# Optimization experiments

Hardware: AMD Instinct MI355X
Metric: run time of the kernel (lower is better)

## Reference

```python
import jax, jax.numpy as jnp
from jax import lax
import numpy as np

DIM = 64
HEADS = 4
R = 8  # reduction_ratio: kv conv kernel == stride == R


def setup_inputs() -> dict:
    key = jax.random.key(0)
    k_x, k_q, k_kv, k_o = jax.random.split(key, 4)
    x = jax.random.normal(k_x, (2, DIM, 32, 64, 64), dtype=jnp.float32)
    # 1x1x1 conv weights stored as [out_c, in_c]
    w_q = jax.random.normal(k_q, (DIM, DIM), dtype=jnp.float32) * (1.0 / np.sqrt(DIM))
    # strided kv conv weights: [out_c=2*dim, in_c=dim, R, R, R]
    fan_in = DIM * R * R * R
    w_kv = jax.random.normal(k_kv, (2 * DIM, DIM, R, R, R), dtype=jnp.float32) * (1.0 / np.sqrt(fan_in))
    w_out = jax.random.normal(k_o, (DIM, DIM), dtype=jnp.float32) * (1.0 / np.sqrt(DIM))
    return {"x": x, "w_q": w_q, "w_kv": w_kv, "w_out": w_out}


def _attn(x, w_q, w_kv, w_out):
    B, C, D, H, W = x.shape
    hd = C // HEADS  # per-head channel dim
    scale = hd ** (-0.5)

    # to_q: 1x1x1 conv == channel mixing
    q = jnp.einsum('oc,bcdhw->bodhw', w_q, x)
    # to_kv: conv3d kernel=stride=R, no padding
    kv = lax.conv_general_dilated(
        x, w_kv, window_strides=(R, R, R), padding='VALID',
        dimension_numbers=('NCDHW', 'OIDHW', 'NCDHW'))
    k, v = jnp.split(kv, 2, axis=1)  # each [B, C, D/R, H/R, W/R]

    def to_seq(t):
        # 'b (h c) d x y -> (b h) (d x y) c'
        b, c_all, d, h, w = t.shape
        t = t.reshape(b, HEADS, hd, d * h * w)
        return t.transpose(0, 1, 3, 2).reshape(b * HEADS, d * h * w, hd)

    qs, ks, vs = to_seq(q), to_seq(k), to_seq(v)  # [(B*H), N, c], [(B*H), Nr, c]

    sim = jnp.einsum('bic,bjc->bij', qs, ks) * scale  # [(B*H), N, Nr]
    attn = jax.nn.softmax(sim, axis=-1)
    out = jnp.einsum('bij,bjc->bic', attn, vs)  # [(B*H), N, c]

    # '(b h) (d x y) c -> b (h c) d x y'
    out = out.reshape(B, HEADS, D * H * W, hd).transpose(0, 1, 3, 2)
    out = out.reshape(B, C, D, H, W)
    return jnp.einsum('oc,bcdhw->bodhw', w_out, out)


def reference(x, w_q, w_kv, w_out):
    return _attn(x, w_q, w_kv, w_out)
```

## Files before the change

kernel.cpp:

```cpp
#include <hip/hip_runtime.h>
#include <hip/hip_bf16.h>

#define NPOS 131072

typedef __attribute__((ext_vector_type(8))) short short8;
typedef __attribute__((ext_vector_type(4))) float floatx4;
typedef unsigned int uint32;

__device__ __forceinline__ unsigned short bf16b(float v) {
    __hip_bfloat16 h = __float2bfloat16(v);
    return __builtin_bit_cast(unsigned short, h);
}
__device__ __forceinline__ uint32 cvtpk(float lo, float hi) {
    uint32 r;
    asm("v_cvt_pk_bf16_f32 %0, %1, %2" : "=v"(r) : "v"(lo), "v"(hi));
    return r;
}
__device__ __forceinline__ uint32 pk2(float lo, float hi) {
    return (uint32)bf16b(lo) | ((uint32)bf16b(hi) << 16);
}
#if __has_builtin(__builtin_amdgcn_exp2f)
#define EXP2(x) __builtin_amdgcn_exp2f(x)
#else
#define EXP2(x) exp2f(x)
#endif
#if __has_builtin(__builtin_amdgcn_rcpf)
#define RCPF(x) __builtin_amdgcn_rcpf(x)
#else
#define RCPF(x) (1.0f / (x))
#endif

__device__ __forceinline__ short8 emb4(uint32 w0, uint32 w1) {
    union { uint32 u[4]; short8 s; } z;
    z.u[0] = w0; z.u[1] = w1; z.u[2] = 0; z.u[3] = 0;
    return z.s;
}
__device__ __forceinline__ short8 emb4m(const unsigned short* p) {
    uint32 w[2];
    __builtin_memcpy(w, p, 8);
    return emb4(w[0], w[1]);
}

__global__ void k_prep_w(const float* __restrict__ wq, const float* __restrict__ wout,
                         unsigned short* __restrict__ wqb, unsigned short* __restrict__ woutb) {
    const float QS = 0.36067376022224085f;
    int gid = blockIdx.x * 256 + threadIdx.x;
    wqb[gid]   = bf16b(wq[gid] * QS);
    woutb[gid] = bf16b(wout[gid]);
}

__global__ void k_prep_wkvb(const float* __restrict__ wkv, unsigned short* __restrict__ wtb) {
    int gid = blockIdx.x * 256 + threadIdx.x;
    int ic = gid >> 14;
    int oc = (gid >> 7) & 127;
    float4 v = *(const float4*)(wkv + ((size_t)(oc * 64 + ic)) * 512 + (size_t)(gid & 127) * 4);
    uint32* dst = (uint32*)(wtb + (size_t)gid * 4);
    dst[0] = cvtpk(v.x, v.y);
    dst[1] = cvtpk(v.z, v.w);
}

__global__ __launch_bounds__(256) void k_conv_mfma(const float* __restrict__ x,
                                                   const unsigned short* __restrict__ wtb,
                                                   float* __restrict__ partial) {
    __shared__ __align__(16) unsigned short As[64 * 72];
    __shared__ __align__(16) unsigned short Bs[128 * 72];
    const int bid = blockIdx.x;
    const int ic = bid & 63;
    const int b  = (bid >> 6) & 1;
    const int pz = bid >> 7;
    const int tid = threadIdx.x;
    const int lane = tid & 63, wv = tid >> 6;
    const int lc = lane & 15, lg = lane >> 4;

    floatx4 acc[4][2];
#pragma unroll
    for (int mt = 0; mt < 4; ++mt)
#pragma unroll
        for (int n = 0; n < 2; ++n) acc[mt][n] = {0.f, 0.f, 0.f, 0.f};

    const float* xp = x + ((size_t)b * 64 + ic) * NPOS + (size_t)pz * 8 * 4096;
    const unsigned short* wp = wtb + (size_t)ic * 128 * 512;

    for (int rz = 0; rz < 8; ++rz) {
        __syncthreads();
        const float* plane = xp + (size_t)rz * 4096;
#pragma unroll
        for (int t2 = 0; t2 < 4; ++t2) {
            int e = (t2 * 256 + tid) * 4;
            int y = e >> 6, x0 = e & 63;
            int p = ((y >> 3) << 3) + (x0 >> 3);
            int k = ((y & 7) << 3) + (x0 & 7);
            float4 v = *(const float4*)(plane + e);
            uint32* dst = (uint32*)&As[p * 72 + k];
            dst[0] = cvtpk(v.x, v.y);
            dst[1] = cvtpk(v.z, v.w);
        }
        {
            int oc = tid >> 1, hf = tid & 1;
            const uint4* src = (const uint4*)(wp + (size_t)oc * 512 + rz * 64 + hf * 32);
            uint4* dst = (uint4*)&Bs[oc * 72 + hf * 32];
#pragma unroll
            for (int r = 0; r < 4; ++r) dst[r] = src[r];
        }
        __syncthreads();
#pragma unroll
        for (int ks = 0; ks < 2; ++ks) {
            short8 bb0 = *(const short8*)&Bs[((wv * 2 + 0) * 16 + lc) * 72 + ks * 32 + lg * 8];
            short8 bb1 = *(const short8*)&Bs[((wv * 2 + 1) * 16 + lc) * 72 + ks * 32 + lg * 8];
#pragma unroll
            for (int mt = 0; mt < 4; ++mt) {
                short8 a = *(const short8*)&As[(mt * 16 + lc) * 72 + ks * 32 + lg * 8];
                acc[mt][0] = __builtin_amdgcn_mfma_f32_16x16x32_bf16(a, bb0, acc[mt][0], 0, 0, 0);
                acc[mt][1] = __builtin_amdgcn_mfma_f32_16x16x32_bf16(a, bb1, acc[mt][1], 0, 0, 0);
            }
        }
    }
    float* pb = partial + (((size_t)ic * 2 + b) * 256 + pz * 64) * 128;
#pragma unroll
    for (int mt = 0; mt < 4; ++mt)
#pragma unroll
        for (int ntl = 0; ntl < 2; ++ntl) {
            int oc = (wv * 2 + ntl) * 16 + lc;
#pragma unroll
            for (int r = 0; r < 4; ++r) {
                int m = mt * 16 + lg * 4 + r;
                pb[(size_t)m * 128 + oc] = acc[mt][ntl][r];
            }
        }
}

__global__ void k_reduce(const float* __restrict__ partial,
                         unsigned short* __restrict__ kt, unsigned short* __restrict__ vt) {
    int gid = blockIdx.x * 256 + threadIdx.x;
    int oc = gid & 127;
    int bp = gid >> 7;
    int b = bp >> 8;
    int j = bp & 255;
    const float* p = partial + (size_t)bp * 128 + oc;
    float s = 0.f;
#pragma unroll 8
    for (int ic = 0; ic < 64; ++ic) s += p[(size_t)ic * 65536];
    int h = (oc & 63) >> 4, i = oc & 15;
    if (oc < 64)
        kt[(((size_t)b * 4 + h) * 256 + j) * 16 + i] = bf16b(s);
    else
        vt[(((size_t)b * 4 + h) * 16 + i) * 256 + j] = bf16b(s);
}

__global__ __launch_bounds__(256, 5) void k_attn13(
    const float* __restrict__ x, const unsigned short* __restrict__ wqb,
    const unsigned short* __restrict__ woutb, const unsigned short* __restrict__ kt,
    const unsigned short* __restrict__ vt, float* __restrict__ out)
{
    __shared__ __align__(16) unsigned short s_at[64 * 72];
    __shared__ __align__(16) unsigned short s_q[4][64 * 20];
    __shared__ float s_l[4][64];

    const int tid = threadIdx.x;
    const int b = blockIdx.x >> 11;
    const int n_base = (blockIdx.x & 2047) << 6;
    const int lane = tid & 63;
    const int wv = tid >> 6;
    const int lc = lane & 15;
    const int lg = lane >> 4;

    unsigned short* qs = s_q[wv];

    {
        int n_l = tid & 63;
        int c0  = (tid >> 6) * 16;
        const float* xb = x + ((size_t)b << 23) + n_base + n_l;
        uint32* xrow = (uint32*)&s_at[n_l * 72 + c0];
#pragma unroll
        for (int r = 0; r < 8; ++r) {
            float v0 = xb[(size_t)(c0 + 2 * r) << 17];
            float v1 = xb[(size_t)(c0 + 2 * r + 1) << 17];
            xrow[r] = cvtpk(v0, v1);
        }
    }
    __syncthreads();

#pragma unroll
    for (int t = 0; t < 4; ++t) {
        floatx4 c = {0.f, 0.f, 0.f, 0.f};
#pragma unroll
        for (int ks = 0; ks < 2; ++ks) {
            short8 a  = *(const short8*)&s_at[(t * 16 + lc) * 72 + ks * 32 + lg * 8];
            short8 bb = emb4m(wqb + (wv * 16 + lc) * 64 + ks * 32 + lg * 8),
                   bf = bb;
            (void)bf;
            short8 bfull;
            __builtin_memcpy(&bfull, wqb + (wv * 16 + lc) * 64 + ks * 32 + lg * 8, 16);
            c = __builtin_amdgcn_mfma_f32_16x16x32_bf16(a, bfull, c, 0, 0, 0);
        }
#pragma unroll
        for (int r = 0; r < 4; ++r)
            qs[(t * 16 + lg * 4 + r) * 20 + lc] = bf16b(c[r]);
    }

    __syncthreads();

    short8 qf[4];
#pragma unroll
    for (int t = 0; t < 4; ++t)
        qf[t] = emb4m(&qs[(t * 16 + lc) * 20 + lg * 4]);

    const unsigned short* kh = kt + (((size_t)b * 4 + wv) << 12);
    const unsigned short* vh = vt + (((size_t)b * 4 + wv) << 12);
    float lp[4] = {0.f, 0.f, 0.f, 0.f};
    floatx4 pv[4];
#pragma unroll
    for (int t = 0; t < 4; ++t) pv[t] = {0.f, 0.f, 0.f, 0.f};

#pragma unroll 4
    for (int jt = 0; jt < 16; ++jt) {
        const int j0 = jt * 16;
        short8 kf = emb4m(kh + (size_t)(j0 + lc) * 16 + lg * 4);
        short8 vf = emb4m(vh + (size_t)lc * 256 + j0 + lg * 4);
#pragma unroll
        for (int t = 0; t < 4; ++t) {
            floatx4 z = {0.f, 0.f, 0.f, 0.f};
            floatx4 c = __builtin_amdgcn_mfma_f32_16x16x32_bf16(kf, qf[t], z, 0, 0, 0);
            float p0 = EXP2(c[0]), p1 = EXP2(c[1]), p2 = EXP2(c[2]), p3 = EXP2(c[3]);
            lp[t] += (p0 + p1) + (p2 + p3);
            short8 pa = emb4(pk2(p0, p1), pk2(p2, p3));
            pv[t] = __builtin_amdgcn_mfma_f32_16x16x32_bf16(pa, vf, pv[t], 0, 0, 0);
        }
    }

#pragma unroll
    for (int t = 0; t < 4; ++t) {
        lp[t] += __shfl_xor(lp[t], 16, 64);
        lp[t] += __shfl_xor(lp[t], 32, 64);
    }
    if (lane < 16) {
#pragma unroll
        for (int t = 0; t < 4; ++t) s_l[wv][t * 16 + lane] = lp[t];
    }
#pragma unroll
    for (int t = 0; t < 4; ++t) {
#pragma unroll
        for (int r = 0; r < 4; ++r) {
            float rl = RCPF(s_l[wv][t * 16 + lg * 4 + r]);
            s_at[(t * 16 + lg * 4 + r) * 72 + wv * 16 + lc] = bf16b(pv[t][r] * rl);
        }
    }

    __syncthreads();

#pragma unroll
    for (int t = 0; t < 4; ++t) {
        floatx4 c = {0.f, 0.f, 0.f, 0.f};
#pragma unroll
        for (int ks = 0; ks < 2; ++ks) {
            short8 a = *(const short8*)&s_at[(t * 16 + lc) * 72 + ks * 32 + lg * 8];
            short8 bfull;
            __builtin_memcpy(&bfull, woutb + (wv * 16 + lc) * 64 + ks * 32 + lg * 8, 16);
            c = __builtin_amdgcn_mfma_f32_16x16x32_bf16(a, bfull, c, 0, 0, 0);
        }
        float* dst = out + ((size_t)b << 23) + (size_t)(wv * 16 + lc) * NPOS
                   + n_base + t * 16 + lg * 4;
        *(floatx4*)dst = c;
    }
}

extern "C" void kernel_launch(void* const* d_in, const int* in_sizes, int n_in,
                              void* d_out, int out_size, void* d_ws, size_t ws_size,
                              hipStream_t stream) {
    const float* x    = (const float*)d_in[0];
    const float* wq   = (const float*)d_in[1];
    const float* wkv  = (const float*)d_in[2];
    const float* wout = (const float*)d_in[3];
    float* out = (float*)d_out;
    float* ws = (float*)d_ws;

    unsigned short* wtb = (unsigned short*)ws;
    float* partial = ws + 2097152;
    unsigned short* ktu = (unsigned short*)(ws + 6291456);
    unsigned short* vtu   = ktu + 32768;
    unsigned short* wqb   = vtu + 32768;
    unsigned short* woutb = wqb + 4096;

    k_prep_w   <<<16,   256, 0, stream>>>(wq, wout, wqb, woutb);
    k_prep_wkvb<<<4096, 256, 0, stream>>>(wkv, wtb);
    k_conv_mfma<<<512,  256, 0, stream>>>(x, wtb, partial);
    k_reduce   <<<256,  256, 0, stream>>>(partial, ktu, vtu);
    k_attn13   <<<4096, 256, 0, stream>>>(x, wqb, woutb, ktu, vtu, out);
}
```

Before: 100.8 us.

## Fill full MFMA K-depth in PV and compute softmax denominator via ones-MFMA

The attention inner loop now handles 32 keys per step. Two QK MFMAs produce a full 8-element P fragment, so the PV MFMA uses its whole K=32 depth instead of half-zero-padded operands. To match the new fragment order, V is stored permuted in the reduce kernel. The softmax row sum is taken by a second MFMA against an all-ones B operand, which replaces the scalar adds, cross-lane shuffles and the shared-memory round trip. A cheaper round-half-up bf16 pack also replaces the library conversion; it trades exact round-to-nearest-even for fewer instructions.

Measured after the change: 93.87 us. -6.9%, faster.

```diff
diff --git a/kernel.cpp b/kernel.cpp
--- a/kernel.cpp
+++ b/kernel.cpp
@@ -16,8 +16,10 @@
     asm("v_cvt_pk_bf16_f32 %0, %1, %2" : "=v"(r) : "v"(lo), "v"(hi));
     return r;
 }
-__device__ __forceinline__ uint32 pk2(float lo, float hi) {
-    return (uint32)bf16b(lo) | ((uint32)bf16b(hi) << 16);
+__device__ __forceinline__ uint32 pkr(float lo, float hi) {
+    uint32 ul = __builtin_bit_cast(uint32, lo) + 0x8000u;
+    uint32 uh = __builtin_bit_cast(uint32, hi) + 0x8000u;
+    return (uh & 0xFFFF0000u) | (ul >> 16);
 }
 #if __has_builtin(__builtin_amdgcn_exp2f)
 #define EXP2(x) __builtin_amdgcn_exp2f(x)
@@ -39,6 +41,11 @@
     uint32 w[2];
     __builtin_memcpy(w, p, 8);
     return emb4(w[0], w[1]);
+}
+__device__ __forceinline__ short8 mk8(uint32 a, uint32 b, uint32 c, uint32 d) {
+    union { uint32 u[4]; short8 s; } z;
+    z.u[0] = a; z.u[1] = b; z.u[2] = c; z.u[3] = d;
+    return z.s;
 }
 
 __global__ void k_prep_w(const float* __restrict__ wq, const float* __restrict__ wout,
@@ -141,20 +148,22 @@
 #pragma unroll 8
     for (int ic = 0; ic < 64; ++ic) s += p[(size_t)ic * 65536];
     int h = (oc & 63) >> 4, i = oc & 15;
-    if (oc < 64)
+    if (oc < 64) {
         kt[(((size_t)b * 4 + h) * 256 + j) * 16 + i] = bf16b(s);
-    else
-        vt[(((size_t)b * 4 + h) * 16 + i) * 256 + j] = bf16b(s);
-}
-
-__global__ __launch_bounds__(256, 5) void k_attn13(
+    } else {
+        int q = j & 31;
+        int jp = (j & ~31) | (((q & 15) >> 2) * 8 + (q & 3) + ((q >> 4) << 2));
+        vt[(((size_t)b * 4 + h) * 16 + i) * 256 + jp] = bf16b(s);
+    }
+}
+
+__global__ __launch_bounds__(256, 5) void k_attn15(
     const float* __restrict__ x, const unsigned short* __restrict__ wqb,
     const unsigned short* __restrict__ woutb, const unsigned short* __restrict__ kt,
     const unsigned short* __restrict__ vt, float* __restrict__ out)
 {
     __shared__ __align__(16) unsigned short s_at[64 * 72];
     __shared__ __align__(16) unsigned short s_q[4][64 * 20];
-    __shared__ float s_l[4][64];
 
     const int tid = threadIdx.x;
     const int b = blockIdx.x >> 11;
@@ -185,10 +194,7 @@
         floatx4 c = {0.f, 0.f, 0.f, 0.f};
 #pragma unroll
         for (int ks = 0; ks < 2; ++ks) {
-            short8 a  = *(const short8*)&s_at[(t * 16 + lc) * 72 + ks * 32 + lg * 8];
-            short8 bb = emb4m(wqb + (wv * 16 + lc) * 64 + ks * 32 + lg * 8),
-                   bf = bb;
-            (void)bf;
+            short8 a = *(const short8*)&s_at[(t * 16 + lc) * 72 + ks * 32 + lg * 8];
             short8 bfull;
             __builtin_memcpy(&bfull, wqb + (wv * 16 + lc) * 64 + ks * 32 + lg * 8, 16);
             c = __builtin_amdgcn_mfma_f32_16x16x32_bf16(a, bfull, c, 0, 0, 0);
@@ -207,41 +213,37 @@
 
     const unsigned short* kh = kt + (((size_t)b * 4 + wv) << 12);
     const unsigned short* vh = vt + (((size_t)b * 4 + wv) << 12);
-    float lp[4] = {0.f, 0.f, 0.f, 0.f};
-    floatx4 pv[4];
-#pragma unroll
-    for (int t = 0; t < 4; ++t) pv[t] = {0.f, 0.f, 0.f, 0.f};
-
-#pragma unroll 4
-    for (int jt = 0; jt < 16; ++jt) {
-        const int j0 = jt * 16;
-        short8 kf = emb4m(kh + (size_t)(j0 + lc) * 16 + lg * 4);
-        short8 vf = emb4m(vh + (size_t)lc * 256 + j0 + lg * 4);
+    const short8 ONES = {(short)0x3F80, (short)0x3F80, (short)0x3F80, (short)0x3F80,
+                         (short)0x3F80, (short)0x3F80, (short)0x3F80, (short)0x3F80};
+    floatx4 pv[4], pvl[4];
+#pragma unroll
+    for (int t = 0; t < 4; ++t) { pv[t] = {0.f, 0.f, 0.f, 0.f}; pvl[t] = {0.f, 0.f, 0.f, 0.f}; }
+
+#pragma unroll 2
+    for (int m = 0; m < 8; ++m) {
+        const int j0 = m * 32;
+        short8 kf0 = emb4m(kh + (size_t)(j0 + lc) * 16 + lg * 4);
+        short8 kf1 = emb4m(kh + (size_t)(j0 + 16 + lc) * 16 + lg * 4);
+        short8 vf;
+        __builtin_memcpy(&vf, vh + (size_t)lc * 256 + j0 + lg * 8, 16);
 #pragma unroll
         for (int t = 0; t < 4; ++t) {
             floatx4 z = {0.f, 0.f, 0.f, 0.f};
-            floatx4 c = __builtin_amdgcn_mfma_f32_16x16x32_bf16(kf, qf[t], z, 0, 0, 0);
-            float p0 = EXP2(c[0]), p1 = EXP2(c[1]), p2 = EXP2(c[2]), p3 = EXP2(c[3]);
-            lp[t] += (p0 + p1) + (p2 + p3);
-            short8 pa = emb4(pk2(p0, p1), pk2(p2, p3));
-            pv[t] = __builtin_amdgcn_mfma_f32_16x16x32_bf16(pa, vf, pv[t], 0, 0, 0);
+            floatx4 c0 = __builtin_amdgcn_mfma_f32_16x16x32_bf16(kf0, qf[t], z, 0, 0, 0);
+            floatx4 c1 = __builtin_amdgcn_mfma_f32_16x16x32_bf16(kf1, qf[t], z, 0, 0, 0);
+            float p0 = EXP2(c0[0]), p1 = EXP2(c0[1]), p2 = EXP2(c0[2]), p3 = EXP2(c0[3]);
+            float p4 = EXP2(c1[0]), p5 = EXP2(c1[1]), p6 = EXP2(c1[2]), p7 = EXP2(c1[3]);
+            short8 pa = mk8(pkr(p0, p1), pkr(p2, p3), pkr(p4, p5), pkr(p6, p7));
+            pv[t]  = __builtin_amdgcn_mfma_f32_16x16x32_bf16(pa, vf,   pv[t],  0, 0, 0);
+            pvl[t] = __builtin_amdgcn_mfma_f32_16x16x32_bf16(pa, ONES, pvl[t], 0, 0, 0);
         }
     }
 
 #pragma unroll
     for (int t = 0; t < 4; ++t) {
-        lp[t] += __shfl_xor(lp[t], 16, 64);
-        lp[t] += __shfl_xor(lp[t], 32, 64);
-    }
-    if (lane < 16) {
-#pragma unroll
-        for (int t = 0; t < 4; ++t) s_l[wv][t * 16 + lane] = lp[t];
-    }
-#pragma unroll
-    for (int t = 0; t < 4; ++t) {
 #pragma unroll
         for (int r = 0; r < 4; ++r) {
-            float rl = RCPF(s_l[wv][t * 16 + lg * 4 + r]);
+            float rl = RCPF(pvl[t][r]);
             s_at[(t * 16 + lg * 4 + r) * 72 + wv * 16 + lc] = bf16b(pv[t][r] * rl);
         }
     }
@@ -285,5 +287,5 @@
     k_prep_wkvb<<<4096, 256, 0, stream>>>(wkv, wtb);
     k_conv_mfma<<<512,  256, 0, stream>>>(x, wtb, partial);
     k_reduce   <<<256,  256, 0, stream>>>(partial, ktu, vtu);
-    k_attn13   <<<4096, 256, 0, stream>>>(x, wqb, woutb, ktu, vtu, out);
-}
+    k_attn15   <<<4096, 256, 0, stream>>>(x, wqb, woutb, ktu, vtu, out);
+}
```
